# Performance work log

Hardware: AMD Instinct MI355X
Metric: run time of the kernel (lower is better)

Reference implementation:

```python
import jax, jax.numpy as jnp
import numpy as np

N_NEURONS = 2048
IN_DIM = 1024
OUT_DIM = 1024
TOKENS = 4096
TIME_STEPS = 3
DENSITY = 0.25


def setup_inputs() -> dict:
    key = jax.random.key(0)
    ks = jax.random.split(key, 10)
    x = jax.random.normal(ks[0], (TOKENS, IN_DIM), dtype=jnp.float32)
    W_in = jax.random.normal(ks[1], (N_NEURONS, IN_DIM), dtype=jnp.float32) * (1.0 / np.sqrt(IN_DIM))
    b_in = jax.random.normal(ks[2], (N_NEURONS,), dtype=jnp.float32) * 0.01
    weights = jax.random.normal(ks[3], (N_NEURONS, N_NEURONS), dtype=jnp.float32) * 0.3
    J = jax.random.normal(ks[4], (N_NEURONS, N_NEURONS), dtype=jnp.float32) * 0.1
    theta = jax.random.uniform(ks[5], (N_NEURONS,), dtype=jnp.float32) * 1.0 + 0.25
    lam = jnp.asarray(0.35, dtype=jnp.float32)
    # connection mask: rand < density, zero diagonal (buffer, fixed)
    m = (jax.random.uniform(ks[6], (N_NEURONS, N_NEURONS)) < DENSITY).astype(jnp.float32)
    mask = m * (1.0 - jnp.eye(N_NEURONS, dtype=jnp.float32))
    noise_raw = jax.random.normal(ks[7], (TIME_STEPS, TOKENS, N_NEURONS), dtype=jnp.float32)
    W_out = jax.random.normal(ks[8], (OUT_DIM, N_NEURONS), dtype=jnp.float32) * (1.0 / np.sqrt(N_NEURONS))
    b_out = jax.random.normal(ks[9], (OUT_DIM,), dtype=jnp.float32) * 0.01
    return {"x": x, "W_in": W_in, "b_in": b_in, "weights": weights, "J": J,
            "theta": theta, "lam": lam, "mask": mask, "noise_raw": noise_raw,
            "W_out": W_out, "b_out": b_out, "time_steps": TIME_STEPS}


def reference(x, W_in, b_in, weights, J, theta, lam, mask, noise_raw, W_out, b_out, time_steps):
    # input projection: [tokens, in_dim] -> [tokens, n]
    state = x @ W_in.T + b_in
    eff_w = weights * mask          # [n, n]
    J_m = J * mask                  # [n, n]
    T = jnp.abs(jnp.sin(2.0 * theta))  # temperature [n]
    for t in range(time_steps):
        signal = state @ eff_w                     # [tokens, n]
        s = jnp.tanh(state)
        # einsum('bi,ij,bj->bj', s, J_m, s) == (s @ J_m) * s
        delta = (s @ J_m) * s                      # [tokens, n]
        noise = noise_raw[t] * T * 0.1             # [tokens, n]
        state = jnp.tanh(signal + lam * delta + noise)
    return state @ W_out.T + b_out
```

## Files before the change

### kernel.cpp

```cpp
#include <hip/hip_runtime.h>
#include <hip/hip_fp16.h>

#define TOKENS 4096
#define NN 2048
#define IN_DIM 1024
#define OUT_DIM 1024
#define TSTEPS 3

typedef _Float16 half8 __attribute__((ext_vector_type(8)));
typedef _Float16 half4 __attribute__((ext_vector_type(4)));
typedef float f32x4 __attribute__((ext_vector_type(4)));

__device__ __forceinline__ void gload_lds16(const void* g, void* l) {
    __builtin_amdgcn_global_load_lds(
        (const __attribute__((address_space(1))) unsigned*)g,
        (__attribute__((address_space(3))) unsigned*)l, 16, 0, 0);
}

#define LGKM(N) asm volatile("s_waitcnt lgkmcnt(" #N ")" ::: "memory")
#define VMCNT(N) asm volatile("s_waitcnt vmcnt(" #N ")" ::: "memory")
#define SCHED0() __builtin_amdgcn_sched_barrier(0)

__global__ __launch_bounds__(512, 2)
void dual_gemm(const _Float16* __restrict__ A0g, const _Float16* __restrict__ B0g,
               _Float16* __restrict__ C0,
               const _Float16* __restrict__ A1g, const _Float16* __restrict__ B1g,
               _Float16* __restrict__ C1)
{
    __shared__ __align__(16) _Float16 lds[2 * 32768];
    const int tid  = threadIdx.x;
    const int wid  = tid >> 6;
    const int lane = tid & 63;

    const int raw  = blockIdx.x;
    const int widx = (raw & 7) * 32 + (raw >> 3);
    const int g    = widx >> 7;
    const int bid  = widx & 127;
    const int by = bid >> 3;
    const int bx = bid & 7;
    const _Float16* __restrict__ A = g ? A1g : A0g;
    const _Float16* __restrict__ B = g ? B1g : B0g;
    _Float16* __restrict__ C = g ? C1 : C0;
    const int brow = by << 8;
    const int bcol = bx << 8;

    const int sr = tid >> 3;
    const int sc = ((tid & 7) ^ (sr & 7)) << 3;
    const _Float16* gA = A + (size_t)(brow + sr) * NN + sc;
    const _Float16* gB = B + (size_t)(bcol + sr) * NN + sc;
    const int ldst = wid << 9;

    auto stA = [&](int T, int h) {
        _Float16* l = lds + (T & 1) * 32768 + h * 8192;
        const _Float16* p = gA + (size_t)(h << 7) * NN + (T << 6);
        gload_lds16(p,           l + ldst);
        gload_lds16(p + 64 * NN, l + 4096 + ldst);
    };
    auto stB = [&](int T, int h) {
        _Float16* l = lds + (T & 1) * 32768 + 16384 + h * 8192;
        const _Float16* p = gB + (size_t)(h << 7) * NN + (T << 6);
        gload_lds16(p,           l + ldst);
        gload_lds16(p + 64 * NN, l + 4096 + ldst);
    };

    const int wr = (wid >> 2) << 7;
    const int wc = (wid & 3) << 6;
    const int lr = lane & 15;
    const int lq = lane >> 4;
    const int x7 = lr & 7;
    const int c0 = (lq ^ x7) << 3;
    const int c1 = ((4 + lq) ^ x7) << 3;
    const int aRow = (wr + lr) << 6;
    const int bRow = 16384 + ((wc + lr) << 6);

    f32x4 acc[8][4];
#pragma unroll
    for (int m = 0; m < 8; ++m)
#pragma unroll
        for (int n = 0; n < 4; ++n) acc[m][n] = (f32x4){0.f, 0.f, 0.f, 0.f};

    half8 a0[8], a1[8], b0[4], b1[4];

    stA(0, 0); stA(0, 1); stB(0, 0); stB(0, 1);
    stA(1, 0); stA(1, 1); stB(1, 0); stB(1, 1);
    VMCNT(8);
    __builtin_amdgcn_s_barrier();
    asm volatile("" ::: "memory");

    for (int T = 0; T < 32; ++T) {
        const _Float16* lb = lds + (T & 1) * 32768;

#pragma unroll
        for (int m = 0; m < 4; ++m) a0[m] = *(const half8*)&lb[aRow + (m << 10) + c0];
#pragma unroll
        for (int n = 0; n < 4; ++n) b0[n] = *(const half8*)&lb[bRow + (n << 10) + c0];
#pragma unroll
        for (int m = 4; m < 8; ++m) a0[m] = *(const half8*)&lb[aRow + (m << 10) + c0];
#pragma unroll
        for (int m = 0; m < 4; ++m) a1[m] = *(const half8*)&lb[aRow + (m << 10) + c1];
#pragma unroll
        for (int n = 0; n < 4; ++n) b1[n] = *(const half8*)&lb[bRow + (n << 10) + c1];
#pragma unroll
        for (int m = 4; m < 8; ++m) a1[m] = *(const half8*)&lb[aRow + (m << 10) + c1];

        LGKM(15);
        SCHED0();
        __builtin_amdgcn_s_setprio(1);
#pragma unroll
        for (int m = 0; m < 4; ++m)
#pragma unroll
            for (int n = 0; n < 4; ++n)
                acc[m][n] = __builtin_amdgcn_mfma_f32_16x16x32_f16(a0[m], b0[n], acc[m][n], 0, 0, 0);
        __builtin_amdgcn_s_setprio(0);
        SCHED0();

        LGKM(12);
        SCHED0();
        __builtin_amdgcn_s_setprio(1);
#pragma unroll
        for (int m = 0; m < 4; ++m)
#pragma unroll
            for (int n = 0; n < 4; ++n)
                acc[m + 4][n] = __builtin_amdgcn_mfma_f32_16x16x32_f16(a0[m + 4], b0[n], acc[m + 4][n], 0, 0, 0);
        __builtin_amdgcn_s_setprio(0);
        SCHED0();

        LGKM(4);
        SCHED0();
        __builtin_amdgcn_s_setprio(1);
#pragma unroll
        for (int m = 0; m < 4; ++m)
#pragma unroll
            for (int n = 0; n < 4; ++n)
                acc[m][n] = __builtin_amdgcn_mfma_f32_16x16x32_f16(a1[m], b1[n], acc[m][n], 0, 0, 0);
        __builtin_amdgcn_s_setprio(0);
        SCHED0();

        LGKM(0);
        __builtin_amdgcn_s_barrier();
        if (T < 30) { stA(T + 2, 0); stA(T + 2, 1); stB(T + 2, 0); stB(T + 2, 1); }
        if (T < 30) { VMCNT(8); }
        else        { VMCNT(0); }
        __builtin_amdgcn_s_barrier();
        asm volatile("" ::: "memory");

        __builtin_amdgcn_s_setprio(1);
#pragma unroll
        for (int m = 0; m < 4; ++m)
#pragma unroll
            for (int n = 0; n < 4; ++n)
                acc[m + 4][n] = __builtin_amdgcn_mfma_f32_16x16x32_f16(a1[m + 4], b1[n], acc[m + 4][n], 0, 0, 0);
        __builtin_amdgcn_s_setprio(0);
        SCHED0();
    }

    const int cr = lq << 2;
    const int cc = lane & 15;
#pragma unroll
    for (int m = 0; m < 8; ++m) {
#pragma unroll
        for (int n = 0; n < 4; ++n) {
            const size_t o0 = (size_t)(brow + wr + m * 16 + cr) * NN
                            + (bcol + wc + n * 16 + cc);
#pragma unroll
            for (int j = 0; j < 4; ++j)
                C[o0 + (size_t)j * NN] = (_Float16)acc[m][n][j];
        }
    }
}

template<int EPI>
__global__ __launch_bounds__(256, 2)
void pgemm(const _Float16* __restrict__ A, const _Float16* __restrict__ B,
           float* __restrict__ Cout, const float* __restrict__ bias,
           _Float16* __restrict__ oSta, _Float16* __restrict__ oS,
           int K, int N, int nbxLog2)
{
    __shared__ __align__(16) _Float16 lds[2 * 16384];
    const int tid  = threadIdx.x;
    const int wid  = tid >> 6;
    const int lane = tid & 63;

    const int raw  = blockIdx.x;
    const int cpx  = gridDim.x >> 3;
    const int widx = (raw & 7) * cpx + (raw >> 3);
    const int by = widx >> nbxLog2;
    const int bx = widx & ((1 << nbxLog2) - 1);
    const int brow = by << 7;
    const int bcol = bx << 7;

    const int sr = tid >> 3;
    const int sc = ((tid & 7) ^ (sr & 7)) << 3;
    const _Float16* gA = A + (size_t)(brow + sr) * K + sc;
    const _Float16* gB = B + (size_t)(bcol + sr) * K + sc;
    const int ldst = wid << 9;

    auto stA = [&](int T) {
        _Float16* l = lds + (T & 1) * 16384;
        const _Float16* p = gA + (T << 6);
#pragma unroll
        for (int r = 0; r < 4; ++r)
            gload_lds16(p + (size_t)(r * 32) * K, l + r * 2048 + ldst);
    };
    auto stB = [&](int T) {
        _Float16* l = lds + (T & 1) * 16384 + 8192;
        const _Float16* p = gB + (T << 6);
#pragma unroll
        for (int r = 0; r < 4; ++r)
            gload_lds16(p + (size_t)(r * 32) * K, l + r * 2048 + ldst);
    };

    const int wr = (wid >> 1) << 6;
    const int wc = (wid & 1) << 6;
    const int lr = lane & 15;
    const int lq = lane >> 4;
    const int x7 = lr & 7;
    const int c0 = (lq ^ x7) << 3;
    const int c1 = ((4 + lq) ^ x7) << 3;
    const int aRow = (wr + lr) << 6;
    const int bRow = 8192 + ((wc + lr) << 6);

    f32x4 acc[4][4];
#pragma unroll
    for (int m = 0; m < 4; ++m)
#pragma unroll
        for (int n = 0; n < 4; ++n) acc[m][n] = (f32x4){0.f, 0.f, 0.f, 0.f};

    half8 af0[4], af1[4], bf0[4], bf1[4];
    const int NT = K >> 6;

    stA(0); stB(0); stA(1); stB(1);
    VMCNT(8);
    __builtin_amdgcn_s_barrier();
    {
        const _Float16* lb = lds;
#pragma unroll
        for (int m = 0; m < 4; ++m) af0[m] = *(const half8*)&lb[aRow + (m << 10) + c0];
#pragma unroll
        for (int n = 0; n < 4; ++n) bf0[n] = *(const half8*)&lb[bRow + (n << 10) + c0];
    }

    for (int T = 0; T < NT; ++T) {
        const _Float16* lb = lds + (T & 1) * 16384;

#pragma unroll
        for (int m = 0; m < 4; ++m) af1[m] = *(const half8*)&lb[aRow + (m << 10) + c1];
#pragma unroll
        for (int n = 0; n < 4; ++n) bf1[n] = *(const half8*)&lb[bRow + (n << 10) + c1];
        LGKM(8);
        SCHED0();
        __builtin_amdgcn_s_setprio(1);
#pragma unroll
        for (int m = 0; m < 4; ++m)
#pragma unroll
            for (int n = 0; n < 4; ++n)
                acc[m][n] = __builtin_amdgcn_mfma_f32_16x16x32_f16(af0[m], bf0[n], acc[m][n], 0, 0, 0);
        __builtin_amdgcn_s_setprio(0);
        SCHED0();

        LGKM(0);
        __builtin_amdgcn_s_barrier();
        if (T < NT - 2) { stA(T + 2); stB(T + 2); VMCNT(8); }
        else if (T == NT - 2) { VMCNT(0); }
        __builtin_amdgcn_s_barrier();
        asm volatile("" ::: "memory");

        if (T < NT - 1) {
            const _Float16* ln = lds + ((T + 1) & 1) * 16384;
#pragma unroll
            for (int m = 0; m < 4; ++m) af0[m] = *(const half8*)&ln[aRow + (m << 10) + c0];
#pragma unroll
            for (int n = 0; n < 4; ++n) bf0[n] = *(const half8*)&ln[bRow + (n << 10) + c0];
        }
        SCHED0();
        __builtin_amdgcn_s_setprio(1);
#pragma unroll
        for (int m = 0; m < 4; ++m)
#pragma unroll
            for (int n = 0; n < 4; ++n)
                acc[m][n] = __builtin_amdgcn_mfma_f32_16x16x32_f16(af1[m], bf1[n], acc[m][n], 0, 0, 0);
        __builtin_amdgcn_s_setprio(0);
        SCHED0();
    }

    const int cr = lq << 2;
    const int cc = lane & 15;
#pragma unroll
    for (int m = 0; m < 4; ++m) {
#pragma unroll
        for (int n = 0; n < 4; ++n) {
            const int ccol = bcol + wc + n * 16 + cc;
#pragma unroll
            for (int j = 0; j < 4; ++j) {
                const int crow = brow + wr + m * 16 + cr + j;
                float v = acc[m][n][j] + bias[ccol];
                const size_t o = (size_t)crow * N + ccol;
                if (EPI == 1) {
                    oSta[o] = (_Float16)v;
                    oS[o] = (_Float16)tanhf(v);
                } else {
                    Cout[o] = v;
                }
            }
        }
    }
}

__global__ void cvt3(const float* __restrict__ s0, _Float16* __restrict__ d0, int n0,
                     const float* __restrict__ s1, _Float16* __restrict__ d1, int n1,
                     const float* __restrict__ s2, _Float16* __restrict__ d2) {
    int i = blockIdx.x * blockDim.x + threadIdx.x;
    const float* src; _Float16* dst; int k;
    if (i < n0)            { src = s0; dst = d0; k = i; }
    else if (i < n0 + n1)  { src = s1; dst = d1; k = i - n0; }
    else                   { src = s2; dst = d2; k = i - n0 - n1; }
    f32x4 v = *(const f32x4*)&src[(size_t)k * 4];
    half4 h;
    h[0] = (_Float16)v[0]; h[1] = (_Float16)v[1];
    h[2] = (_Float16)v[2]; h[3] = (_Float16)v[3];
    *(half4*)&dst[(size_t)k * 4] = h;
}

__global__ void transmul2(const float* __restrict__ W, const float* __restrict__ J,
                          const float* __restrict__ Mk,
                          _Float16* __restrict__ effT, _Float16* __restrict__ JmT) {
    __shared__ float tw[32][33];
    __shared__ float tj[32][33];
    const int bx = blockIdx.x * 32, by = blockIdx.y * 32;
    const int tx = threadIdx.x, ty0 = threadIdx.y;
#pragma unroll
    for (int r = 0; r < 4; ++r) {
        int ty = ty0 + r * 8;
        size_t idx = (size_t)(by + ty) * NN + bx + tx;
        float mv = Mk[idx];
        tw[ty][tx] = W[idx] * mv;
        tj[ty][tx] = J[idx] * mv;
    }
    __syncthreads();
#pragma unroll
    for (int r = 0; r < 4; ++r) {
        int ty = ty0 + r * 8;
        size_t o = (size_t)(bx + ty) * NN + by + tx;
        effT[o] = (_Float16)tw[tx][ty];
        JmT[o]  = (_Float16)tj[tx][ty];
    }
}

__global__ void tsc_kernel(const float* __restrict__ theta, float* __restrict__ Tsc) {
    int i = blockIdx.x * blockDim.x + threadIdx.x;
    if (i < NN) Tsc[i] = fabsf(sinf(2.0f * theta[i])) * 0.1f;
}

__global__ void step_kernel(const _Float16* __restrict__ signalH, const _Float16* __restrict__ sJH,
                            const float* __restrict__ noise, const float* __restrict__ Tsc,
                            const float* __restrict__ lamp,
                            _Float16* __restrict__ stateH, _Float16* __restrict__ sH) {
    const int i4 = blockIdx.x * blockDim.x + threadIdx.x;
    const float lam = lamp[0];
    const size_t base = (size_t)i4 * 4;
    half4 sg = *(const half4*)&signalH[base];
    half4 dj = *(const half4*)&sJH[base];
    f32x4 nz = *(const f32x4*)&noise[base];
    const int col4 = (int)(base & (NN - 1));
    f32x4 tv = *(const f32x4*)&Tsc[col4];
    half4 so = *(const half4*)&sH[base];
    half4 hs, hn;
#pragma unroll
    for (int j = 0; j < 4; ++j) {
        float s = (float)so[j];
        float arg = (float)sg[j] + lam * ((float)dj[j] * s) + nz[j] * tv[j];
        float st = tanhf(arg);
        hs[j] = (_Float16)st;
        hn[j] = (_Float16)tanhf(st);
    }
    *(half4*)&stateH[base] = hs;
    *(half4*)&sH[base] = hn;
}

extern "C" void kernel_launch(void* const* d_in, const int* in_sizes, int n_in,
                              void* d_out, int out_size, void* d_ws, size_t ws_size,
                              hipStream_t stream) {
    const float* x       = (const float*)d_in[0];
    const float* W_in    = (const float*)d_in[1];
    const float* b_in    = (const float*)d_in[2];
    const float* weights = (const float*)d_in[3];
    const float* Jmat    = (const float*)d_in[4];
    const float* theta   = (const float*)d_in[5];
    const float* lam     = (const float*)d_in[6];
    const float* mask    = (const float*)d_in[7];
    const float* noise   = (const float*)d_in[8];
    const float* W_out   = (const float*)d_in[9];
    const float* b_out   = (const float*)d_in[10];
    float* out = (float*)d_out;

    char* w = (char*)d_ws;
    auto alloc = [&](size_t b) { char* p = w; w += (b + 255) & ~(size_t)255; return p; };
    _Float16* xh      = (_Float16*)alloc((size_t)TOKENS * IN_DIM * 2);
    _Float16* WinH    = (_Float16*)alloc((size_t)NN * IN_DIM * 2);
    _Float16* WoutH   = (_Float16*)alloc((size_t)OUT_DIM * NN * 2);
    _Float16* effT    = (_Float16*)alloc((size_t)NN * NN * 2);
    _Float16* JmT     = (_Float16*)alloc((size_t)NN * NN * 2);
    _Float16* stateH  = (_Float16*)alloc((size_t)TOKENS * NN * 2);
    _Float16* sH      = (_Float16*)alloc((size_t)TOKENS * NN * 2);
    _Float16* signalH = (_Float16*)alloc((size_t)TOKENS * NN * 2);
    _Float16* sJH     = (_Float16*)alloc((size_t)TOKENS * NN * 2);
    float* Tsc        = (float*)alloc((size_t)NN * 4);

    const int n0 = TOKENS * IN_DIM / 4;
    const int n1 = NN * IN_DIM / 4;
    const int n2 = OUT_DIM * NN / 4;
    cvt3<<<(n0 + n1 + n2) / 256, 256, 0, stream>>>(x, xh, n0, W_in, WinH, n1, W_out, WoutH);
    transmul2<<<dim3(NN / 32, NN / 32), dim3(32, 8), 0, stream>>>(weights, Jmat, mask, effT, JmT);
    tsc_kernel<<<NN / 256, 256, 0, stream>>>(theta, Tsc);

    pgemm<1><<<(TOKENS / 128) * (NN / 128), 256, 0, stream>>>(
        xh, WinH, nullptr, b_in, stateH, sH, IN_DIM, NN, 4);

    for (int t = 0; t < TSTEPS; ++t) {
        dual_gemm<<<256, 512, 0, stream>>>(stateH, effT, signalH, sH, JmT, sJH);
        step_kernel<<<TOKENS * NN / 4 / 256, 256, 0, stream>>>(
            signalH, sJH, noise + (size_t)t * TOKENS * NN, Tsc, lam, stateH, sH);
    }

    pgemm<2><<<(TOKENS / 128) * (OUT_DIM / 128), 256, 0, stream>>>(
        stateH, WoutH, out, b_out, nullptr, nullptr, NN, OUT_DIM, 3);
}
```

Measured before the change: 339.9 us.

## Fuse both recurrent GEMMs and the tanh step into one kernel

Replaces the dual GEMM plus separate elementwise step kernel with one kernel per time step. Each block computes the state@effW and s@Jm tiles for the same output region with a K-step of 32, then applies the noise, lambda and tanh epilogue directly from registers. State buffers are ping-ponged to avoid read/write hazards. This removes the fp16 signal/sJ intermediates and their round-trips through global memory, as well as one launch per step. In exchange it uses smaller 128x256 tiles with twice as many K iterations and barriers, and the epilogue issues scalar, poorly coalesced loads and stores.

Result: slower. 440.3 us (+29.5%).

```diff
diff --git a/kernel.cpp b/kernel.cpp
--- a/kernel.cpp
+++ b/kernel.cpp
@@ -22,124 +22,96 @@
 #define SCHED0() __builtin_amdgcn_sched_barrier(0)
 
 __global__ __launch_bounds__(512, 2)
-void dual_gemm(const _Float16* __restrict__ A0g, const _Float16* __restrict__ B0g,
-               _Float16* __restrict__ C0,
-               const _Float16* __restrict__ A1g, const _Float16* __restrict__ B1g,
-               _Float16* __restrict__ C1)
+void fused_dual(const _Float16* __restrict__ stateA, const _Float16* __restrict__ sA,
+                const _Float16* __restrict__ effT, const _Float16* __restrict__ JmT,
+                const float* __restrict__ noise, const float* __restrict__ Tsc,
+                const float* __restrict__ lamp,
+                _Float16* __restrict__ stateB, _Float16* __restrict__ sB)
 {
-    __shared__ __align__(16) _Float16 lds[2 * 32768];
+    __shared__ __align__(16) _Float16 lds[2 * 24576];
     const int tid  = threadIdx.x;
     const int wid  = tid >> 6;
     const int lane = tid & 63;
 
     const int raw  = blockIdx.x;
     const int widx = (raw & 7) * 32 + (raw >> 3);
-    const int g    = widx >> 7;
-    const int bid  = widx & 127;
-    const int by = bid >> 3;
-    const int bx = bid & 7;
-    const _Float16* __restrict__ A = g ? A1g : A0g;
-    const _Float16* __restrict__ B = g ? B1g : B0g;
-    _Float16* __restrict__ C = g ? C1 : C0;
-    const int brow = by << 8;
+    const int by = widx >> 3;
+    const int bx = widx & 7;
+    const int brow = by << 7;
     const int bcol = bx << 8;
 
-    const int sr = tid >> 3;
-    const int sc = ((tid & 7) ^ (sr & 7)) << 3;
-    const _Float16* gA = A + (size_t)(brow + sr) * NN + sc;
-    const _Float16* gB = B + (size_t)(bcol + sr) * NN + sc;
+    const int sr = tid >> 2;
+    const int sc = ((tid & 3) ^ ((tid >> 3) & 3)) << 3;
+    const _Float16* gSt = stateA + (size_t)(brow + sr) * NN + sc;
+    const _Float16* gS  = sA     + (size_t)(brow + sr) * NN + sc;
+    const _Float16* gE  = effT   + (size_t)(bcol + sr) * NN + sc;
+    const _Float16* gJ  = JmT    + (size_t)(bcol + sr) * NN + sc;
     const int ldst = wid << 9;
 
-    auto stA = [&](int T, int h) {
-        _Float16* l = lds + (T & 1) * 32768 + h * 8192;
-        const _Float16* p = gA + (size_t)(h << 7) * NN + (T << 6);
-        gload_lds16(p,           l + ldst);
-        gload_lds16(p + 64 * NN, l + 4096 + ldst);
+    auto stage = [&](int T) {
+        _Float16* l = lds + (T & 1) * 24576;
+        const int p = T << 5;
+        gload_lds16(gSt + p,            l + ldst);
+        gload_lds16(gS  + p,            l + 4096  + ldst);
+        gload_lds16(gE  + p,            l + 8192  + ldst);
+        gload_lds16(gE + 128 * NN + p,  l + 12288 + ldst);
+        gload_lds16(gJ  + p,            l + 16384 + ldst);
+        gload_lds16(gJ + 128 * NN + p,  l + 20480 + ldst);
     };
-    auto stB = [&](int T, int h) {
-        _Float16* l = lds + (T & 1) * 32768 + 16384 + h * 8192;
-        const _Float16* p = gB + (size_t)(h << 7) * NN + (T << 6);
-        gload_lds16(p,           l + ldst);
-        gload_lds16(p + 64 * NN, l + 4096 + ldst);
-    };
-
-    const int wr = (wid >> 2) << 7;
+
+    const int wr = (wid >> 2) << 6;
     const int wc = (wid & 3) << 6;
     const int lr = lane & 15;
     const int lq = lane >> 4;
-    const int x7 = lr & 7;
-    const int c0 = (lq ^ x7) << 3;
-    const int c1 = ((4 + lq) ^ x7) << 3;
-    const int aRow = (wr + lr) << 6;
-    const int bRow = 16384 + ((wc + lr) << 6);
-
-    f32x4 acc[8][4];
-#pragma unroll
-    for (int m = 0; m < 8; ++m)
-#pragma unroll
-        for (int n = 0; n < 4; ++n) acc[m][n] = (f32x4){0.f, 0.f, 0.f, 0.f};
-
-    half8 a0[8], a1[8], b0[4], b1[4];
-
-    stA(0, 0); stA(0, 1); stB(0, 0); stB(0, 1);
-    stA(1, 0); stA(1, 1); stB(1, 0); stB(1, 1);
-    VMCNT(8);
+    const int swz = (lq ^ ((lr >> 1) & 3)) << 3;
+    const int aStR = (wr + lr) * 32 + swz;
+    const int aSR  = 4096  + (wr + lr) * 32 + swz;
+    const int bER  = 8192  + (wc + lr) * 32 + swz;
+    const int bJR  = 16384 + (wc + lr) * 32 + swz;
+
+    f32x4 acc1[4][4], acc2[4][4];
+#pragma unroll
+    for (int m = 0; m < 4; ++m)
+#pragma unroll
+        for (int n = 0; n < 4; ++n) {
+            acc1[m][n] = (f32x4){0.f, 0.f, 0.f, 0.f};
+            acc2[m][n] = (f32x4){0.f, 0.f, 0.f, 0.f};
+        }
+
+    half8 a1[4], b1[4], a2[4], b2[4];
+
+    stage(0); stage(1);
+    VMCNT(6);
     __builtin_amdgcn_s_barrier();
     asm volatile("" ::: "memory");
 
-    for (int T = 0; T < 32; ++T) {
-        const _Float16* lb = lds + (T & 1) * 32768;
-
-#pragma unroll
-        for (int m = 0; m < 4; ++m) a0[m] = *(const half8*)&lb[aRow + (m << 10) + c0];
-#pragma unroll
-        for (int n = 0; n < 4; ++n) b0[n] = *(const half8*)&lb[bRow + (n << 10) + c0];
-#pragma unroll
-        for (int m = 4; m < 8; ++m) a0[m] = *(const half8*)&lb[aRow + (m << 10) + c0];
-#pragma unroll
-        for (int m = 0; m < 4; ++m) a1[m] = *(const half8*)&lb[aRow + (m << 10) + c1];
-#pragma unroll
-        for (int n = 0; n < 4; ++n) b1[n] = *(const half8*)&lb[bRow + (n << 10) + c1];
-#pragma unroll
-        for (int m = 4; m < 8; ++m) a1[m] = *(const half8*)&lb[aRow + (m << 10) + c1];
-
-        LGKM(15);
+    for (int T = 0; T < 64; ++T) {
+        const _Float16* lb = lds + (T & 1) * 24576;
+
+#pragma unroll
+        for (int m = 0; m < 4; ++m) a1[m] = *(const half8*)&lb[aStR + (m << 9)];
+#pragma unroll
+        for (int n = 0; n < 4; ++n) b1[n] = *(const half8*)&lb[bER + (n << 9)];
+#pragma unroll
+        for (int m = 0; m < 4; ++m) a2[m] = *(const half8*)&lb[aSR + (m << 9)];
+#pragma unroll
+        for (int n = 0; n < 4; ++n) b2[n] = *(const half8*)&lb[bJR + (n << 9)];
+
+        LGKM(8);
         SCHED0();
         __builtin_amdgcn_s_setprio(1);
 #pragma unroll
         for (int m = 0; m < 4; ++m)
 #pragma unroll
             for (int n = 0; n < 4; ++n)
-                acc[m][n] = __builtin_amdgcn_mfma_f32_16x16x32_f16(a0[m], b0[n], acc[m][n], 0, 0, 0);
-        __builtin_amdgcn_s_setprio(0);
-        SCHED0();
-
-        LGKM(12);
-        SCHED0();
-        __builtin_amdgcn_s_setprio(1);
-#pragma unroll
-        for (int m = 0; m < 4; ++m)
-#pragma unroll
-            for (int n = 0; n < 4; ++n)
-                acc[m + 4][n] = __builtin_amdgcn_mfma_f32_16x16x32_f16(a0[m + 4], b0[n], acc[m + 4][n], 0, 0, 0);
-        __builtin_amdgcn_s_setprio(0);
-        SCHED0();
-
-        LGKM(4);
-        SCHED0();
-        __builtin_amdgcn_s_setprio(1);
-#pragma unroll
-        for (int m = 0; m < 4; ++m)
-#pragma unroll
-            for (int n = 0; n < 4; ++n)
-                acc[m][n] = __builtin_amdgcn_mfma_f32_16x16x32_f16(a1[m], b1[n], acc[m][n], 0, 0, 0);
+                acc1[m][n] = __builtin_amdgcn_mfma_f32_16x16x32_f16(a1[m], b1[n], acc1[m][n], 0, 0, 0);
         __builtin_amdgcn_s_setprio(0);
         SCHED0();
 
         LGKM(0);
         __builtin_amdgcn_s_barrier();
-        if (T < 30) { stA(T + 2, 0); stA(T + 2, 1); stB(T + 2, 0); stB(T + 2, 1); }
-        if (T < 30) { VMCNT(8); }
+        if (T < 62) stage(T + 2);
+        if (T < 62) { VMCNT(6); }
         else        { VMCNT(0); }
         __builtin_amdgcn_s_barrier();
         asm volatile("" ::: "memory");
@@ -149,22 +121,31 @@
         for (int m = 0; m < 4; ++m)
 #pragma unroll
             for (int n = 0; n < 4; ++n)
-                acc[m + 4][n] = __builtin_amdgcn_mfma_f32_16x16x32_f16(a1[m + 4], b1[n], acc[m + 4][n], 0, 0, 0);
+                acc2[m][n] = __builtin_amdgcn_mfma_f32_16x16x32_f16(a2[m], b2[n], acc2[m][n], 0, 0, 0);
         __builtin_amdgcn_s_setprio(0);
         SCHED0();
     }
 
+    const float lam = lamp[0];
     const int cr = lq << 2;
     const int cc = lane & 15;
 #pragma unroll
-    for (int m = 0; m < 8; ++m) {
+    for (int m = 0; m < 4; ++m) {
 #pragma unroll
         for (int n = 0; n < 4; ++n) {
-            const size_t o0 = (size_t)(brow + wr + m * 16 + cr) * NN
-                            + (bcol + wc + n * 16 + cc);
-#pragma unroll
-            for (int j = 0; j < 4; ++j)
-                C[o0 + (size_t)j * NN] = (_Float16)acc[m][n][j];
+            const int ccol = bcol + wc + n * 16 + cc;
+            const float tv = Tsc[ccol];
+#pragma unroll
+            for (int j = 0; j < 4; ++j) {
+                const int crow = brow + wr + m * 16 + cr + j;
+                const size_t o = (size_t)crow * NN + ccol;
+                float s_old = (float)sA[o];
+                float arg = acc1[m][n][j] + lam * (acc2[m][n][j] * s_old)
+                          + noise[o] * tv;
+                float st = tanhf(arg);
+                stateB[o] = (_Float16)st;
+                sB[o]     = (_Float16)tanhf(st);
+            }
         }
     }
 }
@@ -349,32 +330,6 @@
 __global__ void tsc_kernel(const float* __restrict__ theta, float* __restrict__ Tsc) {
     int i = blockIdx.x * blockDim.x + threadIdx.x;
     if (i < NN) Tsc[i] = fabsf(sinf(2.0f * theta[i])) * 0.1f;
-}
-
-__global__ void step_kernel(const _Float16* __restrict__ signalH, const _Float16* __restrict__ sJH,
-                            const float* __restrict__ noise, const float* __restrict__ Tsc,
-                            const float* __restrict__ lamp,
-                            _Float16* __restrict__ stateH, _Float16* __restrict__ sH) {
-    const int i4 = blockIdx.x * blockDim.x + threadIdx.x;
-    const float lam = lamp[0];
-    const size_t base = (size_t)i4 * 4;
-    half4 sg = *(const half4*)&signalH[base];
-    half4 dj = *(const half4*)&sJH[base];
-    f32x4 nz = *(const f32x4*)&noise[base];
-    const int col4 = (int)(base & (NN - 1));
-    f32x4 tv = *(const f32x4*)&Tsc[col4];
-    half4 so = *(const half4*)&sH[base];
-    half4 hs, hn;
-#pragma unroll
-    for (int j = 0; j < 4; ++j) {
-        float s = (float)so[j];
-        float arg = (float)sg[j] + lam * ((float)dj[j] * s) + nz[j] * tv[j];
-        float st = tanhf(arg);
-        hs[j] = (_Float16)st;
-        hn[j] = (_Float16)tanhf(st);
-    }
-    *(half4*)&stateH[base] = hs;
-    *(half4*)&sH[base] = hn;
 }
 
 extern "C" void kernel_launch(void* const* d_in, const int* in_sizes, int n_in,
@@ -395,16 +350,16 @@
 
     char* w = (char*)d_ws;
     auto alloc = [&](size_t b) { char* p = w; w += (b + 255) & ~(size_t)255; return p; };
-    _Float16* xh      = (_Float16*)alloc((size_t)TOKENS * IN_DIM * 2);
-    _Float16* WinH    = (_Float16*)alloc((size_t)NN * IN_DIM * 2);
-    _Float16* WoutH   = (_Float16*)alloc((size_t)OUT_DIM * NN * 2);
-    _Float16* effT    = (_Float16*)alloc((size_t)NN * NN * 2);
-    _Float16* JmT     = (_Float16*)alloc((size_t)NN * NN * 2);
-    _Float16* stateH  = (_Float16*)alloc((size_t)TOKENS * NN * 2);
-    _Float16* sH      = (_Float16*)alloc((size_t)TOKENS * NN * 2);
-    _Float16* signalH = (_Float16*)alloc((size_t)TOKENS * NN * 2);
-    _Float16* sJH     = (_Float16*)alloc((size_t)TOKENS * NN * 2);
-    float* Tsc        = (float*)alloc((size_t)NN * 4);
+    _Float16* xh    = (_Float16*)alloc((size_t)TOKENS * IN_DIM * 2);
+    _Float16* WinH  = (_Float16*)alloc((size_t)NN * IN_DIM * 2);
+    _Float16* WoutH = (_Float16*)alloc((size_t)OUT_DIM * NN * 2);
+    _Float16* effT  = (_Float16*)alloc((size_t)NN * NN * 2);
+    _Float16* JmT   = (_Float16*)alloc((size_t)NN * NN * 2);
+    _Float16* stA   = (_Float16*)alloc((size_t)TOKENS * NN * 2);
+    _Float16* sA    = (_Float16*)alloc((size_t)TOKENS * NN * 2);
+    _Float16* stB   = (_Float16*)alloc((size_t)TOKENS * NN * 2);
+    _Float16* sB    = (_Float16*)alloc((size_t)TOKENS * NN * 2);
+    float* Tsc      = (float*)alloc((size_t)NN * 4);
 
     const int n0 = TOKENS * IN_DIM / 4;
     const int n1 = NN * IN_DIM / 4;
@@ -414,14 +369,16 @@
     tsc_kernel<<<NN / 256, 256, 0, stream>>>(theta, Tsc);
 
     pgemm<1><<<(TOKENS / 128) * (NN / 128), 256, 0, stream>>>(
-        xh, WinH, nullptr, b_in, stateH, sH, IN_DIM, NN, 4);
+        xh, WinH, nullptr, b_in, stA, sA, IN_DIM, NN, 4);
 
     for (int t = 0; t < TSTEPS; ++t) {
-        dual_gemm<<<256, 512, 0, stream>>>(stateH, effT, signalH, sH, JmT, sJH);
-        step_kernel<<<TOKENS * NN / 4 / 256, 256, 0, stream>>>(
-            signalH, sJH, noise + (size_t)t * TOKENS * NN, Tsc, lam, stateH, sH);
+        fused_dual<<<256, 512, 0, stream>>>(
+            stA, sA, effT, JmT, noise + (size_t)t * TOKENS * NN, Tsc, lam, stB, sB);
+        _Float16* tmp;
+        tmp = stA; stA = stB; stB = tmp;
+        tmp = sA;  sA = sB;  sB = tmp;
     }
 
     pgemm<2><<<(TOKENS / 128) * (OUT_DIM / 128), 256, 0, stream>>>(
-        stateH, WoutH, out, b_out, nullptr, nullptr, NN, OUT_DIM, 3);
-}
+        stA, WoutH, out, b_out, nullptr, nullptr, NN, OUT_DIM, 3);
+}
```
